# Performance work log

Hardware: AMD Instinct MI355X
Metric: run time of the kernel (lower is better)

## Reference

```python
import jax, jax.numpy as jnp
import numpy as np

B, N, M, C, H, D = 1, 4096, 4096, 768, 12, 64  # batch, tgt len, src len, in_dim, heads, head_dim
SCALE = D ** -0.5


def setup_inputs() -> dict:
    key = jax.random.key(0)
    ks = jax.random.split(key, 6)
    s = 0.02
    return {
        "x": jax.random.normal(ks[0], (B, N, C), jnp.float32),
        "src": jax.random.normal(ks[1], (B, M, C), jnp.float32),
        "W_qv": jax.random.normal(ks[2], (2 * H * D, C), jnp.float32) * s,
        "W_k": jax.random.normal(ks[3], (H * D, C), jnp.float32) * s,
        "W_proj": jax.random.normal(ks[4], (C, H * D), jnp.float32) * s,
        "b_proj": jnp.zeros((C,), jnp.float32),
    }


def reference(x, src, W_qv, W_k, W_proj, b_proj):
    Bb, Nn, _ = x.shape
    Mm = src.shape[1]
    # q, v come from src; k comes from x (info flows src -> target)
    qv = (src @ W_qv.T).reshape(Bb, Mm, 2, H, D)
    q = qv[:, :, 0].transpose(0, 2, 1, 3)  # (B, H, M, D)
    v = qv[:, :, 1].transpose(0, 2, 1, 3)  # (B, H, M, D)
    k = (x @ W_k.T).reshape(Bb, Nn, H, D) * SCALE  # (B, N, H, D), pre-scaled
    # attn[b,h,n,m] = q[b,h,m,:] . k[b,n,h,:]  (torch: (q @ k).transpose(-2,-1))
    attn = jnp.einsum('bhmd,bnhd->bhnm', q, k)
    attn = jax.nn.softmax(attn, axis=-1)  # softmax over src tokens m
    y = jnp.einsum('bhnm,bhmd->bnhd', attn, v).reshape(Bb, Nn, H * D)
    return y @ W_proj.T + b_proj
```

## Files before the change

kernel.cpp:

```cpp
#include <hip/hip_runtime.h>

using f32x4 = __attribute__((ext_vector_type(4))) float;
using f32x16 = __attribute__((ext_vector_type(16))) float;
using s16x8 = __attribute__((ext_vector_type(8))) short;
using u16x4 = __attribute__((ext_vector_type(4))) unsigned short;
using u32x4 = __attribute__((ext_vector_type(4))) unsigned int;

#define AS1 __attribute__((address_space(1)))
#define AS3 __attribute__((address_space(3)))

__device__ __forceinline__ void gload16(const void* g, void* l) {
  __builtin_amdgcn_global_load_lds((const AS1 unsigned int*)g,
                                   (AS3 unsigned int*)l, 16, 0, 0);
}

__device__ __forceinline__ unsigned short f2bf(float f) {
  unsigned int u = __builtin_bit_cast(unsigned int, f);
  u += 0x7fffu + ((u >> 16) & 1u);
  return (unsigned short)(u >> 16);
}

__device__ __forceinline__ float b2f(unsigned short u) {
  unsigned int x = ((unsigned int)u) << 16;
  return __builtin_bit_cast(float, x);
}

__device__ __forceinline__ unsigned int cvtpk(float lo, float hi) {
  unsigned int w;
  asm("v_cvt_pk_bf16_f32 %0, %1, %2" : "=v"(w) : "v"(lo), "v"(hi));
  return w;
}

__device__ __forceinline__ void plswap(unsigned int& a, unsigned int& b) {
  asm("v_permlane32_swap_b32 %0, %1" : "+v"(a), "+v"(b));
}

__global__ __launch_bounds__(256) void cvt_bf16_multi(
    const float* __restrict__ i0, const float* __restrict__ i1,
    const float* __restrict__ i2, const float* __restrict__ i3,
    const float* __restrict__ i4, unsigned short* __restrict__ o0,
    unsigned short* __restrict__ o1, unsigned short* __restrict__ o2,
    unsigned short* __restrict__ o3, unsigned short* __restrict__ o4) {
  int b = blockIdx.x;
  const float* in;
  unsigned short* out;
  int base, n4;
  if (b < 3072) { in = i0; out = o0; base = b; n4 = 786432; }
  else if (b < 6144) { in = i1; out = o1; base = b - 3072; n4 = 786432; }
  else if (b < 7296) { in = i2; out = o2; base = b - 6144; n4 = 294912; }
  else if (b < 7872) { in = i3; out = o3; base = b - 7296; n4 = 147456; }
  else { in = i4; out = o4; base = b - 7872; n4 = 147456; }
  int i = base * 256 + threadIdx.x;
  if (i >= n4) return;
  f32x4 v = ((const f32x4*)in)[i];
  u16x4 r;
#pragma unroll
  for (int j = 0; j < 4; ++j) r[j] = f2bf(v[j]);
  ((u16x4*)out)[i] = r;
}

__global__ __launch_bounds__(256) void gemm_proj(
    const unsigned short* __restrict__ srcb, const unsigned short* __restrict__ wqvb,
    const unsigned short* __restrict__ xb, const unsigned short* __restrict__ wkb,
    unsigned short* __restrict__ qbuf, unsigned short* __restrict__ vtbuf,
    unsigned short* __restrict__ kbuf) {
  __shared__ __align__(16) unsigned short As[64 * 64];
  __shared__ __align__(16) unsigned short Bs[64 * 64];
  const bool isqv = blockIdx.y < 24;
  const unsigned short* A = isqv ? srcb : xb;
  const unsigned short* B = isqv ? wqvb : wkb;
  const int n0 = (isqv ? blockIdx.y : (blockIdx.y - 24)) * 64;
  const int m0 = blockIdx.x * 64;
  const int t = threadIdx.x;
  const int lane = t & 63;
  const int wid = t >> 6;
  const int wr = wid >> 1, wc = wid & 1;
  const int fr = lane & 15, fq = lane >> 4;

  f32x4 acc[2][2];
#pragma unroll
  for (int i = 0; i < 2; ++i)
#pragma unroll
    for (int j = 0; j < 2; ++j) acc[i][j] = (f32x4){0.f, 0.f, 0.f, 0.f};

  for (int k0 = 0; k0 < 768; k0 += 64) {
#pragma unroll
    for (int p = 0; p < 2; ++p) {
      int idx = p * 256 + t;
      int row = idx >> 3;
      int scb = ((idx & 7) << 4) ^ ((row & 7) << 4);
      char* dstA = (char*)As + (p * 256 + (wid << 6)) * 16;
      char* dstB = (char*)Bs + (p * 256 + (wid << 6)) * 16;
      gload16((const char*)A + (size_t)(m0 + row) * 1536 + (size_t)k0 * 2 + scb, dstA);
      gload16((const char*)B + (size_t)(n0 + row) * 1536 + (size_t)k0 * 2 + scb, dstB);
    }
    __syncthreads();

    s16x8 af[2][2], bfr[2][2];
#pragma unroll
    for (int mi = 0; mi < 2; ++mi)
#pragma unroll
      for (int kk = 0; kk < 2; ++kk) {
        int row = wr * 32 + mi * 16 + fr;
        int cb = (kk * 64 + (fq << 4)) ^ ((row & 7) << 4);
        af[mi][kk] = *(const s16x8*)((const char*)As + row * 128 + cb);
      }
#pragma unroll
    for (int ni = 0; ni < 2; ++ni)
#pragma unroll
      for (int kk = 0; kk < 2; ++kk) {
        int row = wc * 32 + ni * 16 + fr;
        int cb = (kk * 64 + (fq << 4)) ^ ((row & 7) << 4);
        bfr[ni][kk] = *(const s16x8*)((const char*)Bs + row * 128 + cb);
      }
    __builtin_amdgcn_s_setprio(1);
#pragma unroll
    for (int kk = 0; kk < 2; ++kk)
#pragma unroll
      for (int mi = 0; mi < 2; ++mi)
#pragma unroll
        for (int ni = 0; ni < 2; ++ni)
          acc[mi][ni] = __builtin_amdgcn_mfma_f32_16x16x32_bf16(
              af[mi][kk], bfr[ni][kk], acc[mi][ni], 0, 0, 0);
    __builtin_amdgcn_s_setprio(0);
    __syncthreads();
  }

#pragma unroll
  for (int mi = 0; mi < 2; ++mi) {
#pragma unroll
    for (int ni = 0; ni < 2; ++ni) {
      int row0 = m0 + wr * 32 + mi * 16 + (fq << 2);
      int col = n0 + wc * 32 + ni * 16 + fr;
      if (isqv) {
        if (col < 768) {
#pragma unroll
          for (int j = 0; j < 4; ++j)
            qbuf[(size_t)(row0 + j) * 768 + col] = f2bf(acc[mi][ni][j]);
        } else {
          u16x4 pk;
#pragma unroll
          for (int j = 0; j < 4; ++j) pk[j] = f2bf(acc[mi][ni][j]);
          *(u16x4*)(vtbuf + (size_t)(col - 768) * 4096 + row0) = pk;
        }
      } else {
#pragma unroll
        for (int j = 0; j < 4; ++j)
          kbuf[(size_t)(row0 + j) * 768 + col] = f2bf(acc[mi][ni][j] * 0.18033688f);
      }
    }
  }
}

__global__ __launch_bounds__(256) void gemm_out(
    const unsigned short* __restrict__ A, const unsigned short* __restrict__ B,
    float* __restrict__ outp, const float* __restrict__ bias) {
  __shared__ __align__(16) unsigned short As[64 * 64];
  __shared__ __align__(16) unsigned short Bs[64 * 64];
  const int t = threadIdx.x;
  const int lane = t & 63;
  const int wid = t >> 6;
  const int wr = wid >> 1, wc = wid & 1;
  const int m0 = blockIdx.x * 64, n0 = blockIdx.y * 64;
  const int fr = lane & 15, fq = lane >> 4;

  f32x4 acc[2][2];
#pragma unroll
  for (int i = 0; i < 2; ++i)
#pragma unroll
    for (int j = 0; j < 2; ++j) acc[i][j] = (f32x4){0.f, 0.f, 0.f, 0.f};

  for (int k0 = 0; k0 < 768; k0 += 64) {
#pragma unroll
    for (int p = 0; p < 2; ++p) {
      int idx = p * 256 + t;
      int row = idx >> 3;
      int scb = ((idx & 7) << 4) ^ ((row & 7) << 4);
      char* dstA = (char*)As + (p * 256 + (wid << 6)) * 16;
      char* dstB = (char*)Bs + (p * 256 + (wid << 6)) * 16;
      gload16((const char*)A + (size_t)(m0 + row) * 1536 + (size_t)k0 * 2 + scb, dstA);
      gload16((const char*)B + (size_t)(n0 + row) * 1536 + (size_t)k0 * 2 + scb, dstB);
    }
    __syncthreads();

    s16x8 af[2][2], bfr[2][2];
#pragma unroll
    for (int mi = 0; mi < 2; ++mi)
#pragma unroll
      for (int kk = 0; kk < 2; ++kk) {
        int row = wr * 32 + mi * 16 + fr;
        int cb = (kk * 64 + (fq << 4)) ^ ((row & 7) << 4);
        af[mi][kk] = *(const s16x8*)((const char*)As + row * 128 + cb);
      }
#pragma unroll
    for (int ni = 0; ni < 2; ++ni)
#pragma unroll
      for (int kk = 0; kk < 2; ++kk) {
        int row = wc * 32 + ni * 16 + fr;
        int cb = (kk * 64 + (fq << 4)) ^ ((row & 7) << 4);
        bfr[ni][kk] = *(const s16x8*)((const char*)Bs + row * 128 + cb);
      }
    __builtin_amdgcn_s_setprio(1);
#pragma unroll
    for (int kk = 0; kk < 2; ++kk)
#pragma unroll
      for (int mi = 0; mi < 2; ++mi)
#pragma unroll
        for (int ni = 0; ni < 2; ++ni)
          acc[mi][ni] = __builtin_amdgcn_mfma_f32_16x16x32_bf16(
              af[mi][kk], bfr[ni][kk], acc[mi][ni], 0, 0, 0);
    __builtin_amdgcn_s_setprio(0);
    __syncthreads();
  }

#pragma unroll
  for (int mi = 0; mi < 2; ++mi) {
#pragma unroll
    for (int ni = 0; ni < 2; ++ni) {
      int row0 = m0 + wr * 32 + mi * 16 + (fq << 2);
      int col = n0 + wc * 32 + ni * 16 + fr;
      float bv = bias[col];
#pragma unroll
      for (int j = 0; j < 4; ++j)
        outp[(size_t)(row0 + j) * 768 + col] = acc[mi][ni][j] + bv;
    }
  }
}

__global__ __launch_bounds__(256, 3) void attn_kernel(
    const unsigned short* __restrict__ Qk, const unsigned short* __restrict__ Kq,
    const unsigned short* __restrict__ Vt, unsigned short* __restrict__ Po0,
    unsigned short* __restrict__ PoR, float* __restrict__ Pl) {
  __shared__ __align__(16) unsigned short Ks[2][64 * 64];
  __shared__ __align__(16) unsigned short Vs[2][64 * 64];
  const int t = threadIdx.x, lane = t & 63, wid = t >> 6;
  const int half = lane >> 5, l31 = lane & 31;

  int bid = blockIdx.x;
  int f = (bid & 7) * 192 + (bid >> 3);
  const int h = f >> 7;
  const int rem = f & 127;
  const int n0 = (rem >> 2) * 128;
  const int sp = rem & 3;
  const int mbase = sp * 1024;

  s16x8 qf[4];
  {
    const size_t qrow = n0 + wid * 32 + l31;
#pragma unroll
    for (int kc = 0; kc < 4; ++kc)
      qf[kc] = *(const s16x8*)(Qk + qrow * 768 + h * 64 + kc * 16 + half * 8);
  }

  f32x16 o[2];
#pragma unroll
  for (int dt = 0; dt < 2; ++dt)
#pragma unroll
    for (int r = 0; r < 16; ++r) o[dt][r] = 0.f;
  f32x16 lacc;
#pragma unroll
  for (int r = 0; r < 16; ++r) lacc[r] = 0.f;
  f32x16 z16;
#pragma unroll
  for (int r = 0; r < 16; ++r) z16[r] = 0.f;
  s16x8 ones;
#pragma unroll
  for (int i = 0; i < 8; ++i) ones[i] = (short)0x3F80;

  const int rswz = (l31 & 7) << 4;
  const int rbase = l31 * 128;
  int coff[4];
#pragma unroll
  for (int kc = 0; kc < 4; ++kc)
    coff[kc] = (kc * 32 + half * 16) ^ rswz;

  const int srow = t >> 3;
  const int sscb = ((t & 7) << 4) ^ ((srow & 7) << 4);
  const char* kp0 = (const char*)Kq + (size_t)(mbase + srow) * 1536 + h * 128 + sscb;
  const char* kp1 = kp0 + 49152;
  const char* vp0 = (const char*)Vt + (size_t)(h * 64 + srow) * 8192 +
                    (size_t)mbase * 2 + sscb;
  const char* vp1 = vp0 + 262144;
  const int ldst = wid << 10;

  {
    char* kd = (char*)Ks[0] + ldst;
    char* vd = (char*)Vs[0] + ldst;
    gload16(kp0, kd);
    gload16(kp1, kd + 4096);
    gload16(vp0, vd);
    gload16(vp1, vd + 4096);
    kp0 += 98304; kp1 += 98304; vp0 += 128; vp1 += 128;
  }
  asm volatile("s_waitcnt vmcnt(0)" ::: "memory");
  __builtin_amdgcn_s_barrier();
  __builtin_amdgcn_sched_barrier(0);

  for (int it = 0; it < 16; ++it) {
    const int buf = it & 1;
    if (it < 15) {
      char* kd = (char*)Ks[buf ^ 1] + ldst;
      char* vd = (char*)Vs[buf ^ 1] + ldst;
      gload16(kp0, kd);
      gload16(kp1, kd + 4096);
      gload16(vp0, vd);
      gload16(vp1, vd + 4096);
      kp0 += 98304; kp1 += 98304; vp0 += 128; vp1 += 128;
      asm volatile("s_waitcnt vmcnt(4)" ::: "memory");
    } else {
      asm volatile("s_waitcnt vmcnt(0)" ::: "memory");
    }
    __builtin_amdgcn_s_barrier();
    __builtin_amdgcn_sched_barrier(0);

    const char* Ksb = (const char*)Ks[buf];
    const char* Vsb = (const char*)Vs[buf];

    s16x8 pfrag[4];
#pragma unroll
    for (int mt = 0; mt < 2; ++mt) {
      f32x16 s;
      __builtin_amdgcn_s_setprio(1);
      {
        s16x8 kf = *(const s16x8*)(Ksb + mt * 4096 + rbase + coff[0]);
        s = __builtin_amdgcn_mfma_f32_32x32x16_bf16(kf, qf[0], z16, 0, 0, 0);
      }
#pragma unroll
      for (int kc = 1; kc < 4; ++kc) {
        s16x8 kf = *(const s16x8*)(Ksb + mt * 4096 + rbase + coff[kc]);
        s = __builtin_amdgcn_mfma_f32_32x32x16_bf16(kf, qf[kc], s, 0, 0, 0);
      }
      __builtin_amdgcn_s_setprio(0);

#pragma unroll
      for (int r = 0; r < 16; ++r) s[r] = __builtin_exp2f(s[r]);

      unsigned int w[8];
#pragma unroll
      for (int i = 0; i < 8; ++i) w[i] = cvtpk(s[2 * i], s[2 * i + 1]);
      plswap(w[0], w[2]);
      plswap(w[1], w[3]);
      plswap(w[4], w[6]);
      plswap(w[5], w[7]);
      u32x4 f0, f1;
      f0[0] = w[0]; f0[1] = w[1]; f0[2] = w[2]; f0[3] = w[3];
      f1[0] = w[4]; f1[1] = w[5]; f1[2] = w[6]; f1[3] = w[7];
      pfrag[2 * mt] = __builtin_bit_cast(s16x8, f0);
      pfrag[2 * mt + 1] = __builtin_bit_cast(s16x8, f1);

      __builtin_amdgcn_s_setprio(1);
      lacc = __builtin_amdgcn_mfma_f32_32x32x16_bf16(ones, pfrag[2 * mt], lacc, 0, 0, 0);
      lacc = __builtin_amdgcn_mfma_f32_32x32x16_bf16(ones, pfrag[2 * mt + 1], lacc, 0, 0, 0);
      __builtin_amdgcn_s_setprio(0);
    }

    __builtin_amdgcn_s_setprio(1);
#pragma unroll
    for (int dt = 0; dt < 2; ++dt)
#pragma unroll
      for (int kc = 0; kc < 4; ++kc) {
        s16x8 vf = *(const s16x8*)(Vsb + dt * 4096 + rbase + coff[kc]);
        o[dt] = __builtin_amdgcn_mfma_f32_32x32x16_bf16(vf, pfrag[kc], o[dt], 0, 0, 0);
      }
    __builtin_amdgcn_s_setprio(0);
    __builtin_amdgcn_s_barrier();
    __builtin_amdgcn_sched_barrier(0);
  }

  float lsum = lacc[0];
  unsigned short* Po = (sp == 0) ? Po0 : (PoR + (size_t)(sp - 1) * 3145728);
  const size_t n = n0 + wid * 32 + l31;
  if (!half) Pl[sp * 49152 + n * 12 + h] = lsum;
#pragma unroll
  for (int dt = 0; dt < 2; ++dt)
#pragma unroll
    for (int g = 0; g < 4; ++g) {
      u16x4 pk;
#pragma unroll
      for (int e = 0; e < 4; ++e) pk[e] = f2bf(o[dt][4 * g + e]);
      int d = dt * 32 + 8 * g + 4 * half;
      *(u16x4*)(Po + n * 768 + h * 64 + d) = pk;
    }
}

__global__ __launch_bounds__(256) void attn_combine(
    const unsigned short* __restrict__ Po0, const unsigned short* __restrict__ PoR,
    const float* __restrict__ Pl, unsigned short* __restrict__ Y) {
  int idx = blockIdx.x * 256 + threadIdx.x;
  int row = idx / 192;
  int c4 = idx - row * 192;
  int col = c4 * 4;
  int h = col >> 6;
  float l = Pl[(size_t)row * 12 + h] + Pl[49152 + (size_t)row * 12 + h] +
            Pl[2 * 49152 + (size_t)row * 12 + h] +
            Pl[3 * 49152 + (size_t)row * 12 + h];
  float inv = 1.0f / l;
  size_t off = (size_t)row * 768 + col;
  u16x4 a = *(const u16x4*)(Po0 + off);
  u16x4 b = *(const u16x4*)(PoR + off);
  u16x4 c = *(const u16x4*)(PoR + 3145728 + off);
  u16x4 d = *(const u16x4*)(PoR + 2 * 3145728 + off);
  u16x4 r;
#pragma unroll
  for (int e = 0; e < 4; ++e) {
    float s = b2f(a[e]) + b2f(b[e]) + b2f(c[e]) + b2f(d[e]);
    r[e] = f2bf(s * inv);
  }
  *(u16x4*)(Y + (size_t)row * 768 + col) = r;
}

extern "C" void kernel_launch(void* const* d_in, const int* in_sizes, int n_in,
                              void* d_out, int out_size, void* d_ws,
                              size_t ws_size, hipStream_t stream) {
  const float* x = (const float*)d_in[0];
  const float* src = (const float*)d_in[1];
  const float* Wqv = (const float*)d_in[2];
  const float* Wk = (const float*)d_in[3];
  const float* Wp = (const float*)d_in[4];
  const float* bp = (const float*)d_in[5];
  float* out = (float*)d_out;

  char* ws = (char*)d_ws;
  unsigned short* srcb = (unsigned short*)(ws + 0);
  unsigned short* xb   = (unsigned short*)(ws + 6291456);
  unsigned short* wqvb = (unsigned short*)(ws + 12582912);
  unsigned short* wkb  = (unsigned short*)(ws + 14942208);
  unsigned short* wpb  = (unsigned short*)(ws + 16121856);
  unsigned short* qbuf = (unsigned short*)(ws + 17301504);
  unsigned short* vtbuf= (unsigned short*)(ws + 23592960);
  unsigned short* kbuf = (unsigned short*)(ws + 29884416);
  unsigned short* ybuf = (unsigned short*)(ws + 36175872);
  unsigned short* part0 = (unsigned short*)(ws + 0);
  float* lsums = (float*)(ws + 12582912);
  unsigned short* partR = (unsigned short*)(ws + 42467328);

  cvt_bf16_multi<<<8448, 256, 0, stream>>>(src, x, Wqv, Wk, Wp, srcb, xb, wqvb,
                                           wkb, wpb);

  gemm_proj<<<dim3(64, 36), 256, 0, stream>>>(srcb, wqvb, xb, wkb, qbuf, vtbuf,
                                              kbuf);
  attn_kernel<<<1536, 256, 0, stream>>>(kbuf, qbuf, vtbuf, part0, partR, lsums);
  attn_combine<<<3072, 256, 0, stream>>>(part0, partR, lsums, ybuf);
  gemm_out<<<dim3(64, 12), 256, 0, stream>>>(ybuf, wpb, out, bp);
}
```

Before: 138.5 us.

## Fuse split-KV attention combine into output projection GEMM A-tile load

Removes the separate attn_combine kernel and instead merges the four split-KV partial outputs and normalizes by the summed softmax denominators while loading the A tile of the output projection GEMM. The partial sums layout changes to interleave the four splits per (row, head) so one vector load fetches them all. This removes one launch and the Y buffer round trip through memory. In exchange, each of the 12 column blocks of gemm_out recomputes the combine and reads all four partial buffers, and the A tile now uses synchronous loads instead of async global-to-LDS loads.

```diff
diff --git a/kernel.cpp b/kernel.cpp
--- a/kernel.cpp
+++ b/kernel.cpp
@@ -23,6 +23,13 @@
 __device__ __forceinline__ float b2f(unsigned short u) {
   unsigned int x = ((unsigned int)u) << 16;
   return __builtin_bit_cast(float, x);
+}
+
+__device__ __forceinline__ float b2f_lo(unsigned int u) {
+  return __builtin_bit_cast(float, u << 16);
+}
+__device__ __forceinline__ float b2f_hi(unsigned int u) {
+  return __builtin_bit_cast(float, u & 0xffff0000u);
 }
 
 __device__ __forceinline__ unsigned int cvtpk(float lo, float hi) {
@@ -153,7 +160,8 @@
 }
 
 __global__ __launch_bounds__(256) void gemm_out(
-    const unsigned short* __restrict__ A, const unsigned short* __restrict__ B,
+    const unsigned short* __restrict__ Po0, const unsigned short* __restrict__ PoR,
+    const float* __restrict__ Pl, const unsigned short* __restrict__ B,
     float* __restrict__ outp, const float* __restrict__ bias) {
   __shared__ __align__(16) unsigned short As[64 * 64];
   __shared__ __align__(16) unsigned short Bs[64 * 64];
@@ -164,6 +172,9 @@
   const int m0 = blockIdx.x * 64, n0 = blockIdx.y * 64;
   const int fr = lane & 15, fq = lane >> 4;
 
+  const int r0loc = t >> 3;
+  const int ascb = ((t & 7) << 4) ^ ((r0loc & 7) << 4);
+
   f32x4 acc[2][2];
 #pragma unroll
   for (int i = 0; i < 2; ++i)
@@ -171,14 +182,32 @@
     for (int j = 0; j < 2; ++j) acc[i][j] = (f32x4){0.f, 0.f, 0.f, 0.f};
 
   for (int k0 = 0; k0 < 768; k0 += 64) {
+    const int h = k0 >> 6;
+#pragma unroll
+    for (int p = 0; p < 2; ++p) {
+      const int rowg = m0 + p * 32 + r0loc;
+      f32x4 lv = *(const f32x4*)(Pl + ((size_t)rowg * 12 + h) * 4);
+      float inv = 1.0f / (lv[0] + lv[1] + lv[2] + lv[3]);
+      size_t off = (size_t)rowg * 1536 + (size_t)k0 * 2 + ascb;
+      u32x4 a = *(const u32x4*)((const char*)Po0 + off);
+      u32x4 b = *(const u32x4*)((const char*)PoR + off);
+      u32x4 c = *(const u32x4*)((const char*)PoR + 6291456 + off);
+      u32x4 d = *(const u32x4*)((const char*)PoR + 12582912 + off);
+      u32x4 r;
+#pragma unroll
+      for (int e = 0; e < 4; ++e) {
+        float lo = (b2f_lo(a[e]) + b2f_lo(b[e]) + b2f_lo(c[e]) + b2f_lo(d[e])) * inv;
+        float hi = (b2f_hi(a[e]) + b2f_hi(b[e]) + b2f_hi(c[e]) + b2f_hi(d[e])) * inv;
+        r[e] = cvtpk(lo, hi);
+      }
+      *(u32x4*)((char*)As + (p * 256 + t) * 16) = r;
+    }
 #pragma unroll
     for (int p = 0; p < 2; ++p) {
       int idx = p * 256 + t;
       int row = idx >> 3;
       int scb = ((idx & 7) << 4) ^ ((row & 7) << 4);
-      char* dstA = (char*)As + (p * 256 + (wid << 6)) * 16;
       char* dstB = (char*)Bs + (p * 256 + (wid << 6)) * 16;
-      gload16((const char*)A + (size_t)(m0 + row) * 1536 + (size_t)k0 * 2 + scb, dstA);
       gload16((const char*)B + (size_t)(n0 + row) * 1536 + (size_t)k0 * 2 + scb, dstB);
     }
     __syncthreads();
@@ -370,7 +399,7 @@
   float lsum = lacc[0];
   unsigned short* Po = (sp == 0) ? Po0 : (PoR + (size_t)(sp - 1) * 3145728);
   const size_t n = n0 + wid * 32 + l31;
-  if (!half) Pl[sp * 49152 + n * 12 + h] = lsum;
+  if (!half) Pl[(n * 12 + h) * 4 + sp] = lsum;
 #pragma unroll
   for (int dt = 0; dt < 2; ++dt)
 #pragma unroll
@@ -381,32 +410,6 @@
       int d = dt * 32 + 8 * g + 4 * half;
       *(u16x4*)(Po + n * 768 + h * 64 + d) = pk;
     }
-}
-
-__global__ __launch_bounds__(256) void attn_combine(
-    const unsigned short* __restrict__ Po0, const unsigned short* __restrict__ PoR,
-    const float* __restrict__ Pl, unsigned short* __restrict__ Y) {
-  int idx = blockIdx.x * 256 + threadIdx.x;
-  int row = idx / 192;
-  int c4 = idx - row * 192;
-  int col = c4 * 4;
-  int h = col >> 6;
-  float l = Pl[(size_t)row * 12 + h] + Pl[49152 + (size_t)row * 12 + h] +
-            Pl[2 * 49152 + (size_t)row * 12 + h] +
-            Pl[3 * 49152 + (size_t)row * 12 + h];
-  float inv = 1.0f / l;
-  size_t off = (size_t)row * 768 + col;
-  u16x4 a = *(const u16x4*)(Po0 + off);
-  u16x4 b = *(const u16x4*)(PoR + off);
-  u16x4 c = *(const u16x4*)(PoR + 3145728 + off);
-  u16x4 d = *(const u16x4*)(PoR + 2 * 3145728 + off);
-  u16x4 r;
-#pragma unroll
-  for (int e = 0; e < 4; ++e) {
-    float s = b2f(a[e]) + b2f(b[e]) + b2f(c[e]) + b2f(d[e]);
-    r[e] = f2bf(s * inv);
-  }
-  *(u16x4*)(Y + (size_t)row * 768 + col) = r;
 }
 
 extern "C" void kernel_launch(void* const* d_in, const int* in_sizes, int n_in,
@@ -429,7 +432,6 @@
   unsigned short* qbuf = (unsigned short*)(ws + 17301504);
   unsigned short* vtbuf= (unsigned short*)(ws + 23592960);
   unsigned short* kbuf = (unsigned short*)(ws + 29884416);
-  unsigned short* ybuf = (unsigned short*)(ws + 36175872);
   unsigned short* part0 = (unsigned short*)(ws + 0);
   float* lsums = (float*)(ws + 12582912);
   unsigned short* partR = (unsigned short*)(ws + 42467328);
@@ -440,6 +442,5 @@
   gemm_proj<<<dim3(64, 36), 256, 0, stream>>>(srcb, wqvb, xb, wkb, qbuf, vtbuf,
                                               kbuf);
   attn_kernel<<<1536, 256, 0, stream>>>(kbuf, qbuf, vtbuf, part0, partR, lsums);
-  attn_combine<<<3072, 256, 0, stream>>>(part0, partR, lsums, ybuf);
-  gemm_out<<<dim3(64, 12), 256, 0, stream>>>(ybuf, wpb, out, bp);
-}
+  gemm_out<<<dim3(64, 12), 256, 0, stream>>>(part0, partR, lsums, wpb, out, bp);
+}
```

Result: slower. 146.6 us (+5.9%).
